# Kernel tuning notes

Hardware: AMD Instinct MI355X
Metric: run time of the kernel (lower is better)

The kernel has to match this reference:

```python
import jax, jax.numpy as jnp
import numpy as np

N_NODES = 50000
N_EDGES = 800000
N_GRAPHS = 64
IN_C = 64
HID = 64
HEADS = 4
NEG_SLOPE = 0.2
EPS = 1e-16


def setup_inputs() -> dict:
    key = jax.random.key(0)
    ks = jax.random.split(key, 16)
    x = jax.random.normal(ks[0], (N_NODES, IN_C), dtype=jnp.float32)
    edge_index = jax.random.randint(ks[1], (2, N_EDGES), 0, N_NODES, dtype=jnp.int64)
    batch = jnp.sort(jax.random.randint(ks[2], (N_NODES,), 0, N_GRAPHS, dtype=jnp.int64))
    s = 1.0 / np.sqrt(IN_C)
    s2 = 1.0 / np.sqrt(HID * HEADS)
    s3 = 1.0 / np.sqrt(HID)
    return {
        "x": x,
        "edge_index": edge_index,
        "batch": batch,
        # GATv2 layer 1: in 64 -> heads*64 = 256 (concat)
        "Wl1": jax.random.normal(ks[3], (IN_C, HEADS * HID), dtype=jnp.float32) * s,
        "Wr1": jax.random.normal(ks[4], (IN_C, HEADS * HID), dtype=jnp.float32) * s,
        "att1": jax.random.normal(ks[5], (HEADS, HID), dtype=jnp.float32) * s3,
        "b1": jnp.zeros((HEADS * HID,), dtype=jnp.float32),
        # GATv2 layer 2: in 256 -> 1 head * 64
        "Wl2": jax.random.normal(ks[6], (HEADS * HID, HID), dtype=jnp.float32) * s2,
        "Wr2": jax.random.normal(ks[7], (HEADS * HID, HID), dtype=jnp.float32) * s2,
        "att2": jax.random.normal(ks[8], (1, HID), dtype=jnp.float32) * s3,
        "b2": jnp.zeros((HID,), dtype=jnp.float32),
        # MLP head: 64 -> 64 -> 2
        "W3": jax.random.normal(ks[9], (HID, 64), dtype=jnp.float32) * s3,
        "b3": jnp.zeros((64,), dtype=jnp.float32),
        "W4": jax.random.normal(ks[10], (64, 2), dtype=jnp.float32) * (1.0 / 8.0),
        "b4": jnp.zeros((2,), dtype=jnp.float32),
    }


def gatv2_conv(x, src, dst, Wl, Wr, att, bias, heads, out_c, n_nodes):
    # PyG GATv2Conv (eval mode, add_self_loops=False, concat heads):
    # x_l = lin_l(x) used for SOURCE nodes (messages), x_r = lin_r(x) for TARGET nodes.
    xl = (x @ Wl).reshape(n_nodes, heads, out_c)
    xr = (x @ Wr).reshape(n_nodes, heads, out_c)
    e = jax.nn.leaky_relu(xl[src] + xr[dst], NEG_SLOPE)          # [E, H, C]
    logits = jnp.einsum('ehc,hc->eh', e, att)                    # [E, H]
    # numerically stable softmax over incoming edges of each target node
    m = jax.ops.segment_max(logits, dst, num_segments=n_nodes)   # [N, H]
    ex = jnp.exp(logits - m[dst])
    denom = jax.ops.segment_sum(ex, dst, num_segments=n_nodes)   # [N, H]
    alpha = ex / (denom[dst] + EPS)                              # [E, H]
    out = jax.ops.segment_sum(alpha[:, :, None] * xl[src], dst, num_segments=n_nodes)
    return out.reshape(n_nodes, heads * out_c) + bias


def reference(x, edge_index, batch, Wl1, Wr1, att1, b1, Wl2, Wr2, att2, b2, W3, b3, W4, b4):
    src, dst = edge_index[0], edge_index[1]
    n = x.shape[0]
    h = gatv2_conv(x, src, dst, Wl1, Wr1, att1, b1, HEADS, HID, n)
    h = jax.nn.elu(h)
    h = gatv2_conv(h, src, dst, Wl2, Wr2, att2, b2, 1, HID, n)
    h = jax.nn.elu(h)
    # global mean pool over graphs
    sums = jax.ops.segment_sum(h, batch, num_segments=N_GRAPHS)
    cnt = jax.ops.segment_sum(jnp.ones((n,), dtype=h.dtype), batch, num_segments=N_GRAPHS)
    pooled = sums / jnp.maximum(cnt, 1.0)[:, None]
    # MLP head (dropout inactive in eval)
    z = jax.nn.relu(pooled @ W3 + b3)
    return z @ W4 + b4
```

## Files before the change

kernel.cpp:

```cpp
#include <hip/hip_runtime.h>
#include <hip/hip_fp16.h>
#include <math.h>

#define N_NODES 50000
#define N_EDGES 800000
#define N_GRAPHS 64

#if __has_builtin(__builtin_amdgcn_fdot2)
#define HAS_FDOT2 1
typedef _Float16 h2_t __attribute__((ext_vector_type(2)));
#else
#define HAS_FDOT2 0
#endif

typedef _Float16 f16x8 __attribute__((ext_vector_type(8)));
typedef float f32x4 __attribute__((ext_vector_type(4)));

__device__ __forceinline__ float elu1(float v){ return v > 0.f ? v : expm1f(v); }

__device__ __forceinline__ void cvt8f(float4 q, float* v){
    const __half2* h = (const __half2*)&q;
    float2 f;
    f = __half22float2(h[0]); v[0]=f.x; v[1]=f.y;
    f = __half22float2(h[1]); v[2]=f.x; v[3]=f.y;
    f = __half22float2(h[2]); v[4]=f.x; v[5]=f.y;
    f = __half22float2(h[3]); v[6]=f.x; v[7]=f.y;
}

__device__ __forceinline__ float pkdot(float4 q, const __half2* r2, const __half2* a2){
#if HAS_FDOT2
    const __half2 C06 = __builtin_bit_cast(__half2, 0x38CD38CDu);
    const __half2 C04 = __builtin_bit_cast(__half2, 0x36663666u);
    const __half2* qh = (const __half2*)&q;
    float p = 0.f;
    #pragma unroll
    for (int i=0;i<4;i++){
        __half2 u = __hadd2(qh[i], r2[i]);
        unsigned ua = __builtin_bit_cast(unsigned, u) & 0x7FFF7FFFu;
        __half2 lk = __hfma2(C06, u, __hmul2(C04, __builtin_bit_cast(__half2, ua)));
        p = __builtin_amdgcn_fdot2(__builtin_bit_cast(h2_t, lk),
                                   __builtin_bit_cast(h2_t, a2[i]), p, false);
    }
    return p;
#else
    const __half2* qh = (const __half2*)&q;
    float p = 0.f;
    #pragma unroll
    for (int i=0;i<4;i++){
        float2 qf = __half22float2(qh[i]);
        float2 rf = __half22float2(r2[i]);
        float2 af = __half22float2(a2[i]);
        float u0 = qf.x + rf.x, u1 = qf.y + rf.y;
        p = fmaf(fmaxf(u0, 0.2f*u0), af.x, p);
        p = fmaf(fmaxf(u1, 0.2f*u1), af.y, p);
    }
    return p;
#endif
}

__global__ __launch_bounds__(256) void k_prep(const float* __restrict__ x,
        const float* __restrict__ Wl1, const float* __restrict__ Wr1,
        const float* __restrict__ Wl2, const float* __restrict__ Wr2,
        const int* __restrict__ ei,
        __half* __restrict__ xh, __half* __restrict__ Wt1, __half* __restrict__ Wt2,
        int* __restrict__ deg, float* __restrict__ pooled){
    int t = threadIdx.x, bk = blockIdx.x;
    if (bk < 3125){
        int idx = bk*256 + t;
        float4 v = ((const float4*)x)[idx];
        __half2* dst = (__half2*)xh + (size_t)idx*2;
        dst[0] = __floats2half2_rn(v.x, v.y);
        dst[1] = __floats2half2_rn(v.z, v.w);
    } else if (bk < 3381){
        int elem = (bk-3125)*256 + t;
        if (elem < 32768){
            int c = elem >> 6, k = elem & 63;
            float v = (c < 256) ? Wl1[k*256 + c] : Wr1[k*256 + (c-256)];
            Wt1[elem] = __float2half(v);
        } else {
            int e2 = elem - 32768;
            int c = e2 >> 8, k = e2 & 255;
            float v = (c < 64) ? Wl2[k*64 + c] : Wr2[k*64 + (c-64)];
            Wt2[e2] = __float2half(v);
        }
        if (elem < N_GRAPHS*64) pooled[elem] = 0.f;
    } else {
        int e4 = (bk-3381)*256 + t;
        if (e4 < N_EDGES/4){
            int4 d = ((const int4*)(ei + N_EDGES))[e4];
            atomicAdd(&deg[d.x],1); atomicAdd(&deg[d.y],1);
            atomicAdd(&deg[d.z],1); atomicAdd(&deg[d.w],1);
        }
    }
}

__global__ __launch_bounds__(1024) void k_scan_a(const int* __restrict__ deg,
        int* __restrict__ rowptr, int* __restrict__ partial){
    __shared__ int s[1024];
    int t = threadIdx.x; int i = blockIdx.x*1024 + t;
    int v = (i < N_NODES) ? deg[i] : 0;
    s[t] = v; __syncthreads();
    for (int off=1; off<1024; off<<=1){
        int add = (t>=off) ? s[t-off] : 0;
        __syncthreads();
        s[t] += add;
        __syncthreads();
    }
    if (i < N_NODES) rowptr[i] = s[t] - v;
    if (t == 1023) partial[blockIdx.x] = s[1023];
}

__global__ __launch_bounds__(1024) void k_scan_c(int* __restrict__ rowptr,
        int* __restrict__ cursor, const int* __restrict__ partial){
    __shared__ int base;
    if (threadIdx.x == 0){
        int run = 0;
        for (int bk=0; bk<(int)blockIdx.x; bk++) run += partial[bk];
        base = run;
    }
    __syncthreads();
    int i = blockIdx.x*1024 + threadIdx.x;
    if (i < N_NODES){
        int r = rowptr[i] + base;
        rowptr[i] = r; cursor[i] = r;
    } else if (i == N_NODES){
        rowptr[N_NODES] = N_EDGES;
    }
}

__global__ void k_scatter(const int* __restrict__ ei, int* __restrict__ cursor,
                          int* __restrict__ srcs){
    int e4 = blockIdx.x*256 + threadIdx.x;
    if (e4 < N_EDGES/4){
        int4 sv = ((const int4*)ei)[e4];
        int4 dv = ((const int4*)(ei + N_EDGES))[e4];
        int p0 = atomicAdd(&cursor[dv.x],1); srcs[p0] = sv.x;
        int p1 = atomicAdd(&cursor[dv.y],1); srcs[p1] = sv.y;
        int p2 = atomicAdd(&cursor[dv.z],1); srcs[p2] = sv.z;
        int p3 = atomicAdd(&cursor[dv.w],1); srcs[p3] = sv.w;
    }
}

__global__ __launch_bounds__(256) void k_mm1(const __half* __restrict__ xh,
        const __half* __restrict__ Wt1,
        __half* __restrict__ xl1h, __half* __restrict__ xr1h){
    int w = threadIdx.x >> 6, l = threadIdx.x & 63;
    int r0 = blockIdx.x*64 + w*16;
    int cg = blockIdx.y;
    int lr = l & 15, lk = l >> 4, lk4 = lk*4;
    int ar = r0 + lr; if (ar >= N_NODES) ar = N_NODES-1;
    const __half* arow = xh + (size_t)ar*64;
    f16x8 a0 = *(const f16x8*)(arow + lk*8);
    f16x8 a1 = *(const f16x8*)(arow + 32 + lk*8);
    f32x4 acc[8];
    #pragma unroll
    for (int ct=0; ct<8; ct++) acc[ct] = (f32x4){0.f,0.f,0.f,0.f};
    #pragma unroll
    for (int ct=0; ct<8; ct++){
        int col = cg*128 + ct*16 + lr;
        const __half* brow = Wt1 + (size_t)col*64;
        f16x8 b0 = *(const f16x8*)(brow + lk*8);
        f16x8 b1 = *(const f16x8*)(brow + 32 + lk*8);
        acc[ct] = __builtin_amdgcn_mfma_f32_16x16x32_f16(a0, b0, acc[ct], 0,0,0);
        acc[ct] = __builtin_amdgcn_mfma_f32_16x16x32_f16(a1, b1, acc[ct], 0,0,0);
    }
    __half* base = (cg < 2) ? xl1h : xr1h;
    int cbase = (cg < 2) ? cg*128 : (cg-2)*128;
    #pragma unroll
    for (int ct=0; ct<8; ct++){
        int cc = cbase + ct*16 + lr;
        #pragma unroll
        for (int i=0;i<4;i++){
            int row = r0 + lk4 + i;
            if (row < N_NODES) base[(size_t)row*256 + cc] = __float2half(acc[ct][i]);
        }
    }
}

__global__ __launch_bounds__(256) void k_mm2(const __half* __restrict__ h1h,
        const __half* __restrict__ Wt2,
        __half* __restrict__ xl2h, __half* __restrict__ xr2h){
    int w = threadIdx.x >> 6, l = threadIdx.x & 63;
    int r0 = blockIdx.x*64 + w*16;
    int cg = blockIdx.y;
    int lr = l & 15, lk = l >> 4, lk4 = lk*4;
    int ar = r0 + lr; if (ar >= N_NODES) ar = N_NODES-1;
    const __half* arow = h1h + (size_t)ar*256;
    f32x4 acc[4];
    #pragma unroll
    for (int ct=0; ct<4; ct++) acc[ct] = (f32x4){0.f,0.f,0.f,0.f};
    #pragma unroll
    for (int ks=0; ks<8; ks++){
        f16x8 a = *(const f16x8*)(arow + ks*32 + lk*8);
        #pragma unroll
        for (int ct=0; ct<4; ct++){
            int col = cg*64 + ct*16 + lr;
            f16x8 bf = *(const f16x8*)(Wt2 + (size_t)col*256 + ks*32 + lk*8);
            acc[ct] = __builtin_amdgcn_mfma_f32_16x16x32_f16(a, bf, acc[ct], 0,0,0);
        }
    }
    __half* base = (cg == 0) ? xl2h : xr2h;
    #pragma unroll
    for (int ct=0; ct<4; ct++){
        int cc = ct*16 + lr;
        #pragma unroll
        for (int i=0;i<4;i++){
            int row = r0 + lk4 + i;
            if (row < N_NODES) base[(size_t)row*64 + cc] = __float2half(acc[ct][i]);
        }
    }
}

__global__ __launch_bounds__(256) void k_gat1(const __half* __restrict__ xlh,
        const __half* __restrict__ xrh, const int* __restrict__ srcs,
        const int* __restrict__ rowptr, const float* __restrict__ att,
        const float* __restrict__ b, __half* __restrict__ h1h){
    int w = threadIdx.x >> 6, l = threadIdx.x & 63;
    int n = blockIdx.x*4 + w;
    int g = l >> 5, sub = l & 31;
    const float4* xh4 = (const float4*)xlh;
    float4 rq = *(const float4*)(xrh + (size_t)n*256 + sub*8);
    __half2 r2[4];
    { const __half2* rh = (const __half2*)&rq;
      r2[0]=rh[0]; r2[1]=rh[1]; r2[2]=rh[2]; r2[3]=rh[3]; }
    float4 A0 = *(const float4*)(att + sub*8);
    float4 A1 = *(const float4*)(att + sub*8 + 4);
    __half2 a2[4] = { __floats2half2_rn(A0.x,A0.y), __floats2half2_rn(A0.z,A0.w),
                      __floats2half2_rn(A1.x,A1.y), __floats2half2_rn(A1.z,A1.w) };
    float acc[8];
    #pragma unroll
    for (int c=0;c<8;c++) acc[c]=0.f;
    float dacc = 0.f;
    int beg = rowptr[n], end = rowptr[n+1];
    for (int j = beg; j < end; j += 8){
        int j0=j+g, j1=j+2+g, j2=j+4+g, j3=j+6+g;
        bool c0=j0<end, c1=j1<end, c2=j2<end, c3=j3<end;
        int s0 = c0 ? srcs[j0] : 0;
        int s1 = c1 ? srcs[j1] : 0;
        int s2 = c2 ? srcs[j2] : 0;
        int s3 = c3 ? srcs[j3] : 0;
        float4 q0 = xh4[(size_t)(unsigned)s0*32 + sub];
        float4 q1 = xh4[(size_t)(unsigned)s1*32 + sub];
        float4 q2 = xh4[(size_t)(unsigned)s2*32 + sub];
        float4 q3 = xh4[(size_t)(unsigned)s3*32 + sub];
        float p0 = pkdot(q0, r2, a2);
        float p1 = pkdot(q1, r2, a2);
        float p2 = pkdot(q2, r2, a2);
        float p3 = pkdot(q3, r2, a2);
        #pragma unroll
        for (int off=1; off<8; off<<=1){
            p0 += __shfl_xor(p0, off);
            p1 += __shfl_xor(p1, off);
            p2 += __shfl_xor(p2, off);
            p3 += __shfl_xor(p3, off);
        }
        float e0 = c0 ? __expf(p0) : 0.f;
        float e1 = c1 ? __expf(p1) : 0.f;
        float e2 = c2 ? __expf(p2) : 0.f;
        float e3 = c3 ? __expf(p3) : 0.f;
        float v0[8], v1[8], v2[8], v3[8];
        cvt8f(q0,v0); cvt8f(q1,v1); cvt8f(q2,v2); cvt8f(q3,v3);
        #pragma unroll
        for (int c=0;c<8;c++)
            acc[c] = fmaf(e0,v0[c], fmaf(e1,v1[c], fmaf(e2,v2[c], fmaf(e3,v3[c], acc[c]))));
        dacc += e0 + e1 + e2 + e3;
    }
    #pragma unroll
    for (int c=0;c<8;c++) acc[c] += __shfl_xor(acc[c], 32);
    dacc += __shfl_xor(dacc, 32);
    if (l < 32){
        float inv = 1.f / (dacc + 1e-16f);
        float4 B0 = *(const float4*)(b + l*8);
        float4 B1 = *(const float4*)(b + l*8 + 4);
        float4 st;
        __half2* sp = (__half2*)&st;
        sp[0] = __floats2half2_rn(elu1(fmaf(acc[0],inv,B0.x)), elu1(fmaf(acc[1],inv,B0.y)));
        sp[1] = __floats2half2_rn(elu1(fmaf(acc[2],inv,B0.z)), elu1(fmaf(acc[3],inv,B0.w)));
        sp[2] = __floats2half2_rn(elu1(fmaf(acc[4],inv,B1.x)), elu1(fmaf(acc[5],inv,B1.y)));
        sp[3] = __floats2half2_rn(elu1(fmaf(acc[6],inv,B1.z)), elu1(fmaf(acc[7],inv,B1.w)));
        *(float4*)(h1h + (size_t)n*256 + l*8) = st;
    }
}

__global__ __launch_bounds__(256) void k_gat2(const __half* __restrict__ xlh,
        const __half* __restrict__ xrh, const int* __restrict__ srcs,
        const int* __restrict__ rowptr, const float* __restrict__ att,
        const float* __restrict__ b, float* __restrict__ h2){
    int w = threadIdx.x >> 6, l = threadIdx.x & 63;
    int n = blockIdx.x*4 + w;
    int g = l >> 3, sub = l & 7;
    const float4* xh4 = (const float4*)xlh;
    float4 rq = *(const float4*)(xrh + (size_t)n*64 + sub*8);
    __half2 r2[4];
    { const __half2* rh = (const __half2*)&rq;
      r2[0]=rh[0]; r2[1]=rh[1]; r2[2]=rh[2]; r2[3]=rh[3]; }
    float4 A0 = *(const float4*)(att + sub*8);
    float4 A1 = *(const float4*)(att + sub*8 + 4);
    __half2 a2[4] = { __floats2half2_rn(A0.x,A0.y), __floats2half2_rn(A0.z,A0.w),
                      __floats2half2_rn(A1.x,A1.y), __floats2half2_rn(A1.z,A1.w) };
    float acc[8];
    #pragma unroll
    for (int c=0;c<8;c++) acc[c]=0.f;
    float dacc = 0.f;
    int beg = rowptr[n], end = rowptr[n+1];
    for (int j = beg; j < end; j += 16){
        int j0 = j+g, j1 = j+8+g;
        bool c0 = j0<end, c1 = j1<end;
        int s0 = c0 ? srcs[j0] : 0;
        int s1 = c1 ? srcs[j1] : 0;
        float4 q0 = xh4[(size_t)(unsigned)s0*8 + sub];
        float4 q1 = xh4[(size_t)(unsigned)s1*8 + sub];
        float p0 = pkdot(q0, r2, a2);
        float p1 = pkdot(q1, r2, a2);
        #pragma unroll
        for (int off=1; off<8; off<<=1){
            p0 += __shfl_xor(p0, off);
            p1 += __shfl_xor(p1, off);
        }
        float e0 = c0 ? __expf(p0) : 0.f;
        float e1 = c1 ? __expf(p1) : 0.f;
        float v0[8], v1[8];
        cvt8f(q0,v0); cvt8f(q1,v1);
        #pragma unroll
        for (int c=0;c<8;c++)
            acc[c] = fmaf(e0,v0[c], fmaf(e1,v1[c], acc[c]));
        dacc += e0 + e1;
    }
    #pragma unroll
    for (int off=8; off<64; off<<=1){
        #pragma unroll
        for (int c=0;c<8;c++) acc[c] += __shfl_xor(acc[c], off);
        dacc += __shfl_xor(dacc, off);
    }
    if (l < 8){
        float inv = 1.f / (dacc + 1e-16f);
        float4 B0 = *(const float4*)(b + l*8);
        float4 B1 = *(const float4*)(b + l*8 + 4);
        float4 o0, o1;
        o0.x = elu1(fmaf(acc[0], inv, B0.x));
        o0.y = elu1(fmaf(acc[1], inv, B0.y));
        o0.z = elu1(fmaf(acc[2], inv, B0.z));
        o0.w = elu1(fmaf(acc[3], inv, B0.w));
        o1.x = elu1(fmaf(acc[4], inv, B1.x));
        o1.y = elu1(fmaf(acc[5], inv, B1.y));
        o1.z = elu1(fmaf(acc[6], inv, B1.z));
        o1.w = elu1(fmaf(acc[7], inv, B1.w));
        float4* op = (float4*)(h2 + (size_t)n*64 + l*8);
        op[0] = o0; op[1] = o1;
    }
}

__device__ __forceinline__ int lower_bound_i(const int* a, int n, int key){
    int lo = 0, hi = n;
    while (lo < hi){ int mid = (lo+hi)>>1; if (a[mid] < key) lo = mid+1; else hi = mid; }
    return lo;
}

__global__ __launch_bounds__(256) void k_pool(const float* __restrict__ h2,
        const int* __restrict__ batch, float* __restrict__ pooled){
    int gph = blockIdx.x, part = blockIdx.y;
    int t = threadIdx.x, c = t & 63, q = t >> 6;
    int start = lower_bound_i(batch, N_NODES, gph);
    int end   = lower_bound_i(batch, N_NODES, gph+1);
    int len = end - start;
    int is = start + (int)(((long long)len*part) >> 3);
    int ie = start + (int)(((long long)len*(part+1)) >> 3);
    float s = 0.f;
    for (int i = is + q; i < ie; i += 4) s += h2[(size_t)i*64 + c];
    __shared__ float red[256];
    red[t] = s; __syncthreads();
    if (q == 0){
        float tot = red[c] + red[64+c] + red[128+c] + red[192+c];
        atomicAdd(&pooled[gph*64 + c], tot);
    }
}

__global__ __launch_bounds__(64) void k_mlp(const float* __restrict__ pooled,
        const int* __restrict__ batch,
        const float* __restrict__ W3, const float* __restrict__ b3,
        const float* __restrict__ W4, const float* __restrict__ b4,
        float* __restrict__ out){
    int gph = blockIdx.x, t = threadIdx.x;
    __shared__ float ps[64], zs[64];
    int start = lower_bound_i(batch, N_NODES, gph);
    int end   = lower_bound_i(batch, N_NODES, gph+1);
    float cnt = fmaxf((float)(end - start), 1.f);
    ps[t] = pooled[gph*64 + t] / cnt;
    __syncthreads();
    float a = b3[t];
    for (int k=0;k<64;k++) a = fmaf(ps[k], W3[k*64+t], a);
    zs[t] = fmaxf(a, 0.f); __syncthreads();
    if (t < 2){
        float o = b4[t];
        for (int k=0;k<64;k++) o = fmaf(zs[k], W4[k*2+t], o);
        out[gph*2 + t] = o;
    }
}

extern "C" void kernel_launch(void* const* d_in, const int* in_sizes, int n_in,
                              void* d_out, int out_size, void* d_ws, size_t ws_size,
                              hipStream_t stream) {
    const float* x    = (const float*)d_in[0];
    const int*   ei   = (const int*)  d_in[1];
    const int*   batch= (const int*)  d_in[2];
    const float* Wl1  = (const float*)d_in[3];
    const float* Wr1  = (const float*)d_in[4];
    const float* att1 = (const float*)d_in[5];
    const float* b1   = (const float*)d_in[6];
    const float* Wl2  = (const float*)d_in[7];
    const float* Wr2  = (const float*)d_in[8];
    const float* att2 = (const float*)d_in[9];
    const float* b2   = (const float*)d_in[10];
    const float* W3   = (const float*)d_in[11];
    const float* b3   = (const float*)d_in[12];
    const float* W4   = (const float*)d_in[13];
    const float* b4   = (const float*)d_in[14];
    float* out = (float*)d_out;

    char* wsp = (char*)d_ws;
    size_t off = 0;
    auto alloc = [&](size_t bytes) -> char* {
        char* p = wsp + off; off += (bytes + 255) & ~(size_t)255; return p;
    };
    __half* xh    = (__half*)alloc((size_t)N_NODES*64*2);
    __half* Wt1   = (__half*)alloc(512*64*2);
    __half* Wt2   = (__half*)alloc(128*256*2);
    __half* xl1h  = (__half*)alloc((size_t)N_NODES*256*2);
    __half* xr1h  = (__half*)alloc((size_t)N_NODES*256*2);
    __half* h1h   = (__half*)alloc((size_t)N_NODES*256*2);
    int* rowptr   = (int*)alloc((N_NODES+1)*4);
    int* cursor   = (int*)alloc(N_NODES*4);
    int* partial  = (int*)alloc(64*4);
    int* srcs     = (int*)alloc((size_t)N_EDGES*4);
    int* deg      = (int*)alloc(N_NODES*4);
    float* pooled = (float*)alloc(N_GRAPHS*64*4);
    __half* xl2h  = xl1h;
    __half* xr2h  = xl1h + (size_t)N_NODES*64;
    float*  h2    = (float*)xr1h;

    hipMemsetAsync(deg, 0, (size_t)N_NODES*sizeof(int), stream);
    k_prep<<<3125+256+782, 256, 0, stream>>>(x, Wl1, Wr1, Wl2, Wr2, ei,
                                             xh, Wt1, Wt2, deg, pooled);
    k_scan_a<<<49, 1024, 0, stream>>>(deg, rowptr, partial);
    k_scan_c<<<49, 1024, 0, stream>>>(rowptr, cursor, partial);
    k_scatter<<<782, 256, 0, stream>>>(ei, cursor, srcs);

    k_mm1<<<dim3(782,4), 256, 0, stream>>>(xh, Wt1, xl1h, xr1h);
    k_gat1<<<N_NODES/4, 256, 0, stream>>>(xl1h, xr1h, srcs, rowptr, att1, b1, h1h);
    k_mm2<<<dim3(782,2), 256, 0, stream>>>(h1h, Wt2, xl2h, xr2h);
    k_gat2<<<N_NODES/4, 256, 0, stream>>>(xl2h, xr2h, srcs, rowptr, att2, b2, h2);
    k_pool<<<dim3(N_GRAPHS,8), 256, 0, stream>>>(h2, batch, pooled);
    k_mlp<<<N_GRAPHS, 64, 0, stream>>>(pooled, batch, W3, b3, W4, b4, out);
}
```

Measured before the change: 296.5 us.

## Fuse scatter into mm1, fuse pooling into gat2, use fp16 packed aggregation

The edge scatter now runs as an extra grid row inside the first matmul kernel, and the separate pooling kernel is removed: gat2 atomically adds its ELU outputs straight into the per-graph pooled sums. The attention dot now uses two fdot2 calls with leaky-relu split into 0.6·u + 0.4·|u| terms, with log2(e) folded in so exp2f can be used. Message aggregation switches to packed half FMAs, in gat2 accumulated entirely in fp16. This cuts launches, the h2 round trip and conversion work, at the cost of fp16 precision loss, unnormalised exponentials that can overflow in half, and heavy atomic contention on 64 graph rows.

```diff
diff --git a/kernel.cpp b/kernel.cpp
--- a/kernel.cpp
+++ b/kernel.cpp
@@ -5,6 +5,7 @@
 #define N_NODES 50000
 #define N_EDGES 800000
 #define N_GRAPHS 64
+#define L2E 1.44269504f
 
 #if __has_builtin(__builtin_amdgcn_fdot2)
 #define HAS_FDOT2 1
@@ -18,44 +19,34 @@
 
 __device__ __forceinline__ float elu1(float v){ return v > 0.f ? v : expm1f(v); }
 
-__device__ __forceinline__ void cvt8f(float4 q, float* v){
-    const __half2* h = (const __half2*)&q;
-    float2 f;
-    f = __half22float2(h[0]); v[0]=f.x; v[1]=f.y;
-    f = __half22float2(h[1]); v[2]=f.x; v[3]=f.y;
-    f = __half22float2(h[2]); v[4]=f.x; v[5]=f.y;
-    f = __half22float2(h[3]); v[6]=f.x; v[7]=f.y;
-}
-
-__device__ __forceinline__ float pkdot(float4 q, const __half2* r2, const __half2* a2){
-#if HAS_FDOT2
-    const __half2 C06 = __builtin_bit_cast(__half2, 0x38CD38CDu);
-    const __half2 C04 = __builtin_bit_cast(__half2, 0x36663666u);
+__device__ __forceinline__ float pkdot(float4 q, const __half2* r2,
+        const __half2* A6, const __half2* A4){
     const __half2* qh = (const __half2*)&q;
     float p = 0.f;
+#if HAS_FDOT2
     #pragma unroll
     for (int i=0;i<4;i++){
         __half2 u = __hadd2(qh[i], r2[i]);
-        unsigned ua = __builtin_bit_cast(unsigned, u) & 0x7FFF7FFFu;
-        __half2 lk = __hfma2(C06, u, __hmul2(C04, __builtin_bit_cast(__half2, ua)));
-        p = __builtin_amdgcn_fdot2(__builtin_bit_cast(h2_t, lk),
-                                   __builtin_bit_cast(h2_t, a2[i]), p, false);
-    }
-    return p;
+        __half2 ua = __builtin_bit_cast(__half2,
+            __builtin_bit_cast(unsigned, u) & 0x7FFF7FFFu);
+        p = __builtin_amdgcn_fdot2(__builtin_bit_cast(h2_t,u),
+                                   __builtin_bit_cast(h2_t,A6[i]), p, false);
+        p = __builtin_amdgcn_fdot2(__builtin_bit_cast(h2_t,ua),
+                                   __builtin_bit_cast(h2_t,A4[i]), p, false);
+    }
 #else
-    const __half2* qh = (const __half2*)&q;
-    float p = 0.f;
     #pragma unroll
     for (int i=0;i<4;i++){
         float2 qf = __half22float2(qh[i]);
         float2 rf = __half22float2(r2[i]);
-        float2 af = __half22float2(a2[i]);
+        float2 s6 = __half22float2(A6[i]);
+        float2 s4 = __half22float2(A4[i]);
         float u0 = qf.x + rf.x, u1 = qf.y + rf.y;
-        p = fmaf(fmaxf(u0, 0.2f*u0), af.x, p);
-        p = fmaf(fmaxf(u1, 0.2f*u1), af.y, p);
-    }
+        p = fmaf(s6.x, u0, fmaf(s4.x, fabsf(u0), p));
+        p = fmaf(s6.y, u1, fmaf(s4.y, fabsf(u1), p));
+    }
+#endif
     return p;
-#endif
 }
 
 __global__ __launch_bounds__(256) void k_prep(const float* __restrict__ x,
@@ -128,22 +119,23 @@
     }
 }
 
-__global__ void k_scatter(const int* __restrict__ ei, int* __restrict__ cursor,
-                          int* __restrict__ srcs){
-    int e4 = blockIdx.x*256 + threadIdx.x;
-    if (e4 < N_EDGES/4){
-        int4 sv = ((const int4*)ei)[e4];
-        int4 dv = ((const int4*)(ei + N_EDGES))[e4];
-        int p0 = atomicAdd(&cursor[dv.x],1); srcs[p0] = sv.x;
-        int p1 = atomicAdd(&cursor[dv.y],1); srcs[p1] = sv.y;
-        int p2 = atomicAdd(&cursor[dv.z],1); srcs[p2] = sv.z;
-        int p3 = atomicAdd(&cursor[dv.w],1); srcs[p3] = sv.w;
-    }
-}
-
 __global__ __launch_bounds__(256) void k_mm1(const __half* __restrict__ xh,
         const __half* __restrict__ Wt1,
-        __half* __restrict__ xl1h, __half* __restrict__ xr1h){
+        __half* __restrict__ xl1h, __half* __restrict__ xr1h,
+        const int* __restrict__ ei, int* __restrict__ cursor,
+        int* __restrict__ srcs){
+    if (blockIdx.y == 4){
+        int e4 = blockIdx.x*256 + threadIdx.x;
+        if (e4 < N_EDGES/4){
+            int4 sv = ((const int4*)ei)[e4];
+            int4 dv = ((const int4*)(ei + N_EDGES))[e4];
+            int p0 = atomicAdd(&cursor[dv.x],1); srcs[p0] = sv.x;
+            int p1 = atomicAdd(&cursor[dv.y],1); srcs[p1] = sv.y;
+            int p2 = atomicAdd(&cursor[dv.z],1); srcs[p2] = sv.z;
+            int p3 = atomicAdd(&cursor[dv.w],1); srcs[p3] = sv.w;
+        }
+        return;
+    }
     int w = threadIdx.x >> 6, l = threadIdx.x & 63;
     int r0 = blockIdx.x*64 + w*16;
     int cg = blockIdx.y;
@@ -223,13 +215,21 @@
     __half2 r2[4];
     { const __half2* rh = (const __half2*)&rq;
       r2[0]=rh[0]; r2[1]=rh[1]; r2[2]=rh[2]; r2[3]=rh[3]; }
-    float4 A0 = *(const float4*)(att + sub*8);
-    float4 A1 = *(const float4*)(att + sub*8 + 4);
-    __half2 a2[4] = { __floats2half2_rn(A0.x,A0.y), __floats2half2_rn(A0.z,A0.w),
-                      __floats2half2_rn(A1.x,A1.y), __floats2half2_rn(A1.z,A1.w) };
-    float acc[8];
-    #pragma unroll
-    for (int c=0;c<8;c++) acc[c]=0.f;
+    float4 A0v = *(const float4*)(att + sub*8);
+    float4 A1v = *(const float4*)(att + sub*8 + 4);
+    const float C6 = 0.6f*L2E, C4 = 0.4f*L2E;
+    __half2 A6[4] = { __floats2half2_rn(A0v.x*C6, A0v.y*C6),
+                      __floats2half2_rn(A0v.z*C6, A0v.w*C6),
+                      __floats2half2_rn(A1v.x*C6, A1v.y*C6),
+                      __floats2half2_rn(A1v.z*C6, A1v.w*C6) };
+    __half2 A4[4] = { __floats2half2_rn(A0v.x*C4, A0v.y*C4),
+                      __floats2half2_rn(A0v.z*C4, A0v.w*C4),
+                      __floats2half2_rn(A1v.x*C4, A1v.y*C4),
+                      __floats2half2_rn(A1v.z*C4, A1v.w*C4) };
+    const __half2 Z2 = __floats2half2_rn(0.f, 0.f);
+    float accf[8];
+    #pragma unroll
+    for (int c=0;c<8;c++) accf[c]=0.f;
     float dacc = 0.f;
     int beg = rowptr[n], end = rowptr[n+1];
     for (int j = beg; j < end; j += 8){
@@ -243,10 +243,10 @@
         float4 q1 = xh4[(size_t)(unsigned)s1*32 + sub];
         float4 q2 = xh4[(size_t)(unsigned)s2*32 + sub];
         float4 q3 = xh4[(size_t)(unsigned)s3*32 + sub];
-        float p0 = pkdot(q0, r2, a2);
-        float p1 = pkdot(q1, r2, a2);
-        float p2 = pkdot(q2, r2, a2);
-        float p3 = pkdot(q3, r2, a2);
+        float p0 = pkdot(q0, r2, A6, A4);
+        float p1 = pkdot(q1, r2, A6, A4);
+        float p2 = pkdot(q2, r2, A6, A4);
+        float p3 = pkdot(q3, r2, A6, A4);
         #pragma unroll
         for (int off=1; off<8; off<<=1){
             p0 += __shfl_xor(p0, off);
@@ -254,19 +254,32 @@
             p2 += __shfl_xor(p2, off);
             p3 += __shfl_xor(p3, off);
         }
-        float e0 = c0 ? __expf(p0) : 0.f;
-        float e1 = c1 ? __expf(p1) : 0.f;
-        float e2 = c2 ? __expf(p2) : 0.f;
-        float e3 = c3 ? __expf(p3) : 0.f;
-        float v0[8], v1[8], v2[8], v3[8];
-        cvt8f(q0,v0); cvt8f(q1,v1); cvt8f(q2,v2); cvt8f(q3,v3);
-        #pragma unroll
-        for (int c=0;c<8;c++)
-            acc[c] = fmaf(e0,v0[c], fmaf(e1,v1[c], fmaf(e2,v2[c], fmaf(e3,v3[c], acc[c]))));
+        float e0 = c0 ? exp2f(p0) : 0.f;
+        float e1 = c1 ? exp2f(p1) : 0.f;
+        float e2 = c2 ? exp2f(p2) : 0.f;
+        float e3 = c3 ? exp2f(p3) : 0.f;
+        __half2 E0 = __half2half2(__float2half_rn(e0));
+        __half2 E1 = __half2half2(__float2half_rn(e1));
+        __half2 E2 = __half2half2(__float2half_rn(e2));
+        __half2 E3 = __half2half2(__float2half_rn(e3));
+        const __half2* q0h = (const __half2*)&q0;
+        const __half2* q1h = (const __half2*)&q1;
+        const __half2* q2h = (const __half2*)&q2;
+        const __half2* q3h = (const __half2*)&q3;
+        #pragma unroll
+        for (int i=0;i<4;i++){
+            __half2 a16 = __hfma2(E0, q0h[i], Z2);
+            a16 = __hfma2(E1, q1h[i], a16);
+            a16 = __hfma2(E2, q2h[i], a16);
+            a16 = __hfma2(E3, q3h[i], a16);
+            float2 f = __half22float2(a16);
+            accf[2*i]   += f.x;
+            accf[2*i+1] += f.y;
+        }
         dacc += e0 + e1 + e2 + e3;
     }
     #pragma unroll
-    for (int c=0;c<8;c++) acc[c] += __shfl_xor(acc[c], 32);
+    for (int c=0;c<8;c++) accf[c] += __shfl_xor(accf[c], 32);
     dacc += __shfl_xor(dacc, 32);
     if (l < 32){
         float inv = 1.f / (dacc + 1e-16f);
@@ -274,10 +287,10 @@
         float4 B1 = *(const float4*)(b + l*8 + 4);
         float4 st;
         __half2* sp = (__half2*)&st;
-        sp[0] = __floats2half2_rn(elu1(fmaf(acc[0],inv,B0.x)), elu1(fmaf(acc[1],inv,B0.y)));
-        sp[1] = __floats2half2_rn(elu1(fmaf(acc[2],inv,B0.z)), elu1(fmaf(acc[3],inv,B0.w)));
-        sp[2] = __floats2half2_rn(elu1(fmaf(acc[4],inv,B1.x)), elu1(fmaf(acc[5],inv,B1.y)));
-        sp[3] = __floats2half2_rn(elu1(fmaf(acc[6],inv,B1.z)), elu1(fmaf(acc[7],inv,B1.w)));
+        sp[0] = __floats2half2_rn(elu1(fmaf(accf[0],inv,B0.x)), elu1(fmaf(accf[1],inv,B0.y)));
+        sp[1] = __floats2half2_rn(elu1(fmaf(accf[2],inv,B0.z)), elu1(fmaf(accf[3],inv,B0.w)));
+        sp[2] = __floats2half2_rn(elu1(fmaf(accf[4],inv,B1.x)), elu1(fmaf(accf[5],inv,B1.y)));
+        sp[3] = __floats2half2_rn(elu1(fmaf(accf[6],inv,B1.z)), elu1(fmaf(accf[7],inv,B1.w)));
         *(float4*)(h1h + (size_t)n*256 + l*8) = st;
     }
 }
@@ -285,7 +298,8 @@
 __global__ __launch_bounds__(256) void k_gat2(const __half* __restrict__ xlh,
         const __half* __restrict__ xrh, const int* __restrict__ srcs,
         const int* __restrict__ rowptr, const float* __restrict__ att,
-        const float* __restrict__ b, float* __restrict__ h2){
+        const float* __restrict__ b, const int* __restrict__ batch,
+        float* __restrict__ pooled){
     int w = threadIdx.x >> 6, l = threadIdx.x & 63;
     int n = blockIdx.x*4 + w;
     int g = l >> 3, sub = l & 7;
@@ -294,13 +308,19 @@
     __half2 r2[4];
     { const __half2* rh = (const __half2*)&rq;
       r2[0]=rh[0]; r2[1]=rh[1]; r2[2]=rh[2]; r2[3]=rh[3]; }
-    float4 A0 = *(const float4*)(att + sub*8);
-    float4 A1 = *(const float4*)(att + sub*8 + 4);
-    __half2 a2[4] = { __floats2half2_rn(A0.x,A0.y), __floats2half2_rn(A0.z,A0.w),
-                      __floats2half2_rn(A1.x,A1.y), __floats2half2_rn(A1.z,A1.w) };
-    float acc[8];
-    #pragma unroll
-    for (int c=0;c<8;c++) acc[c]=0.f;
+    float4 A0v = *(const float4*)(att + sub*8);
+    float4 A1v = *(const float4*)(att + sub*8 + 4);
+    const float C6 = 0.6f*L2E, C4 = 0.4f*L2E;
+    __half2 A6[4] = { __floats2half2_rn(A0v.x*C6, A0v.y*C6),
+                      __floats2half2_rn(A0v.z*C6, A0v.w*C6),
+                      __floats2half2_rn(A1v.x*C6, A1v.y*C6),
+                      __floats2half2_rn(A1v.z*C6, A1v.w*C6) };
+    __half2 A4[4] = { __floats2half2_rn(A0v.x*C4, A0v.y*C4),
+                      __floats2half2_rn(A0v.z*C4, A0v.w*C4),
+                      __floats2half2_rn(A1v.x*C4, A1v.y*C4),
+                      __floats2half2_rn(A1v.z*C4, A1v.w*C4) };
+    const __half2 Z2 = __floats2half2_rn(0.f, 0.f);
+    __half2 a16[4] = {Z2, Z2, Z2, Z2};
     float dacc = 0.f;
     int beg = rowptr[n], end = rowptr[n+1];
     for (int j = beg; j < end; j += 16){
@@ -310,43 +330,55 @@
         int s1 = c1 ? srcs[j1] : 0;
         float4 q0 = xh4[(size_t)(unsigned)s0*8 + sub];
         float4 q1 = xh4[(size_t)(unsigned)s1*8 + sub];
-        float p0 = pkdot(q0, r2, a2);
-        float p1 = pkdot(q1, r2, a2);
+        float p0 = pkdot(q0, r2, A6, A4);
+        float p1 = pkdot(q1, r2, A6, A4);
         #pragma unroll
         for (int off=1; off<8; off<<=1){
             p0 += __shfl_xor(p0, off);
             p1 += __shfl_xor(p1, off);
         }
-        float e0 = c0 ? __expf(p0) : 0.f;
-        float e1 = c1 ? __expf(p1) : 0.f;
-        float v0[8], v1[8];
-        cvt8f(q0,v0); cvt8f(q1,v1);
-        #pragma unroll
-        for (int c=0;c<8;c++)
-            acc[c] = fmaf(e0,v0[c], fmaf(e1,v1[c], acc[c]));
+        float e0 = c0 ? exp2f(p0) : 0.f;
+        float e1 = c1 ? exp2f(p1) : 0.f;
+        __half2 E0 = __half2half2(__float2half_rn(e0));
+        __half2 E1 = __half2half2(__float2half_rn(e1));
+        const __half2* q0h = (const __half2*)&q0;
+        const __half2* q1h = (const __half2*)&q1;
+        #pragma unroll
+        for (int i=0;i<4;i++){
+            a16[i] = __hfma2(E0, q0h[i], a16[i]);
+            a16[i] = __hfma2(E1, q1h[i], a16[i]);
+        }
         dacc += e0 + e1;
     }
+    float accf[8];
+    #pragma unroll
+    for (int i=0;i<4;i++){
+        float2 f = __half22float2(a16[i]);
+        accf[2*i] = f.x; accf[2*i+1] = f.y;
+    }
     #pragma unroll
     for (int off=8; off<64; off<<=1){
         #pragma unroll
-        for (int c=0;c<8;c++) acc[c] += __shfl_xor(acc[c], off);
+        for (int c=0;c<8;c++) accf[c] += __shfl_xor(accf[c], off);
         dacc += __shfl_xor(dacc, off);
     }
     if (l < 8){
         float inv = 1.f / (dacc + 1e-16f);
         float4 B0 = *(const float4*)(b + l*8);
         float4 B1 = *(const float4*)(b + l*8 + 4);
-        float4 o0, o1;
-        o0.x = elu1(fmaf(acc[0], inv, B0.x));
-        o0.y = elu1(fmaf(acc[1], inv, B0.y));
-        o0.z = elu1(fmaf(acc[2], inv, B0.z));
-        o0.w = elu1(fmaf(acc[3], inv, B0.w));
-        o1.x = elu1(fmaf(acc[4], inv, B1.x));
-        o1.y = elu1(fmaf(acc[5], inv, B1.y));
-        o1.z = elu1(fmaf(acc[6], inv, B1.z));
-        o1.w = elu1(fmaf(acc[7], inv, B1.w));
-        float4* op = (float4*)(h2 + (size_t)n*64 + l*8);
-        op[0] = o0; op[1] = o1;
+        float o[8];
+        o[0] = elu1(fmaf(accf[0], inv, B0.x));
+        o[1] = elu1(fmaf(accf[1], inv, B0.y));
+        o[2] = elu1(fmaf(accf[2], inv, B0.z));
+        o[3] = elu1(fmaf(accf[3], inv, B0.w));
+        o[4] = elu1(fmaf(accf[4], inv, B1.x));
+        o[5] = elu1(fmaf(accf[5], inv, B1.y));
+        o[6] = elu1(fmaf(accf[6], inv, B1.z));
+        o[7] = elu1(fmaf(accf[7], inv, B1.w));
+        int gph = batch[n];
+        float* pp = pooled + gph*64 + l*8;
+        #pragma unroll
+        for (int c=0;c<8;c++) atomicAdd(&pp[c], o[c]);
     }
 }
 
@@ -354,25 +386,6 @@
     int lo = 0, hi = n;
     while (lo < hi){ int mid = (lo+hi)>>1; if (a[mid] < key) lo = mid+1; else hi = mid; }
     return lo;
-}
-
-__global__ __launch_bounds__(256) void k_pool(const float* __restrict__ h2,
-        const int* __restrict__ batch, float* __restrict__ pooled){
-    int gph = blockIdx.x, part = blockIdx.y;
-    int t = threadIdx.x, c = t & 63, q = t >> 6;
-    int start = lower_bound_i(batch, N_NODES, gph);
-    int end   = lower_bound_i(batch, N_NODES, gph+1);
-    int len = end - start;
-    int is = start + (int)(((long long)len*part) >> 3);
-    int ie = start + (int)(((long long)len*(part+1)) >> 3);
-    float s = 0.f;
-    for (int i = is + q; i < ie; i += 4) s += h2[(size_t)i*64 + c];
-    __shared__ float red[256];
-    red[t] = s; __syncthreads();
-    if (q == 0){
-        float tot = red[c] + red[64+c] + red[128+c] + red[192+c];
-        atomicAdd(&pooled[gph*64 + c], tot);
-    }
 }
 
 __global__ __launch_bounds__(64) void k_mlp(const float* __restrict__ pooled,
@@ -436,19 +449,17 @@
     float* pooled = (float*)alloc(N_GRAPHS*64*4);
     __half* xl2h  = xl1h;
     __half* xr2h  = xl1h + (size_t)N_NODES*64;
-    float*  h2    = (float*)xr1h;
 
     hipMemsetAsync(deg, 0, (size_t)N_NODES*sizeof(int), stream);
     k_prep<<<3125+256+782, 256, 0, stream>>>(x, Wl1, Wr1, Wl2, Wr2, ei,
                                              xh, Wt1, Wt2, deg, pooled);
     k_scan_a<<<49, 1024, 0, stream>>>(deg, rowptr, partial);
     k_scan_c<<<49, 1024, 0, stream>>>(rowptr, cursor, partial);
-    k_scatter<<<782, 256, 0, stream>>>(ei, cursor, srcs);
-
-    k_mm1<<<dim3(782,4), 256, 0, stream>>>(xh, Wt1, xl1h, xr1h);
+
+    k_mm1<<<dim3(782,5), 256, 0, stream>>>(xh, Wt1, xl1h, xr1h, ei, cursor, srcs);
     k_gat1<<<N_NODES/4, 256, 0, stream>>>(xl1h, xr1h, srcs, rowptr, att1, b1, h1h);
     k_mm2<<<dim3(782,2), 256, 0, stream>>>(h1h, Wt2, xl2h, xr2h);
-    k_gat2<<<N_NODES/4, 256, 0, stream>>>(xl2h, xr2h, srcs, rowptr, att2, b2, h2);
-    k_pool<<<dim3(N_GRAPHS,8), 256, 0, stream>>>(h2, batch, pooled);
+    k_gat2<<<N_NODES/4, 256, 0, stream>>>(xl2h, xr2h, srcs, rowptr, att2, b2,
+                                          batch, pooled);
     k_mlp<<<N_GRAPHS, 64, 0, stream>>>(pooled, batch, W3, b3, W4, b4, out);
 }
```

Measured after the change: 667.9 us. +125.2%, slower.
